# Kernel optimization log

Measured on AMD Instinct MI355X. Metric: run time of the kernel, lower is better.

The kernel has to match this reference:

```python
import jax, jax.numpy as jnp
import numpy as np

DIM = 768
NUM_SS = 8
INNER = DIM // 4  # s_ratio = 4 -> 192


def setup_inputs() -> dict:
    key = jax.random.key(0)
    ks = jax.random.split(key, 9)
    s = 0.02
    return {
        "x": jax.random.normal(ks[0], (16, 4096, DIM), dtype=jnp.float32),
        "Wq": jax.random.normal(ks[1], (DIM, DIM), dtype=jnp.float32) * s,
        "bq": jax.random.normal(ks[2], (DIM,), dtype=jnp.float32) * s,
        "Wk": jax.random.normal(ks[3], (DIM, NUM_SS * INNER), dtype=jnp.float32) * s,
        "bk": jax.random.normal(ks[4], (NUM_SS * INNER,), dtype=jnp.float32) * s,
        "Wv": jax.random.normal(ks[5], (DIM, DIM), dtype=jnp.float32) * s,
        "bv": jax.random.normal(ks[6], (DIM,), dtype=jnp.float32) * s,
        "Wss_out": jax.random.normal(ks[7], (INNER, DIM), dtype=jnp.float32) * s,
        "bss_out": jax.random.normal(ks[8], (DIM,), dtype=jnp.float32) * s,
    }


def reference(x, Wq, bq, Wk, bk, Wv, bv, Wss_out, bss_out):
    b = x.shape[0]
    ss_tokens = x[:, -NUM_SS:, :]          # [b, S, D]
    reg = x[:, :-NUM_SS, :]                # [b, T, D]
    x_v = reg @ Wv + bv                    # [b, T, D]
    x_q = reg @ Wq + bq                    # [b, T, D]
    x_k = reg @ Wk + bk                    # [b, T, S*I]
    # mean over regular tokens, reshape to one inner vector per ss token
    ss_update_ = jnp.mean(x_k, axis=1).reshape(b, NUM_SS, INNER)
    new_ss = ss_tokens + (ss_update_ @ Wss_out + bss_out)     # [b, S, D]
    scale = jnp.asarray(1.0 / np.sqrt(DIM), x.dtype)
    sim = jnp.einsum('btd,bsd->bts', x_q, new_ss) * scale     # [b, T, S]
    attn = jax.nn.softmax(sim, axis=-1)
    upd = jnp.einsum('bts,bsd->btd', attn, new_ss)            # [b, T, D]
    new_reg = jax.nn.relu(x_v + upd)
    return jnp.concatenate([new_reg, new_ss], axis=1)
```

## Files before the change

### kernel.cpp

```cpp
#include <hip/hip_runtime.h>
#include <hip/hip_bf16.h>

#define B_ 16
#define T_ 4096
#define TREG 4088
#define D_ 768
#define NSS 8
#define INNER_ 192
#define NK 1536
#define NCHUNK 128

typedef unsigned int u32;
typedef unsigned short u16;
typedef __attribute__((ext_vector_type(8))) short bf16x8;
typedef __attribute__((ext_vector_type(4))) float f32x4;

__device__ __forceinline__ u16 f2bf(float f) {
  union { __hip_bfloat16 h; u16 u; } cv;
  cv.h = __float2bfloat16(f);
  return cv.u;
}

__device__ __forceinline__ void load16_lds(const void* g, void* l) {
  __builtin_amdgcn_global_load_lds(
      (const __attribute__((address_space(1))) u32*)(unsigned long long)g,
      (__attribute__((address_space(3))) u32*)(u32)(unsigned long long)l,
      16, 0, 0);
}

__global__ __launch_bounds__(256) void k_wvt(const float* __restrict__ Wv,
                                             u16* __restrict__ wvT) {
  __shared__ float tile[16][17];
  int tx = threadIdx.x & 15, ty = threadIdx.x >> 4;
  int nb = blockIdx.x * 16, kb = blockIdx.y * 16;
  tile[ty][tx] = Wv[(size_t)(kb + ty) * D_ + nb + tx];
  __syncthreads();
  wvT[(size_t)(nb + ty) * D_ + kb + tx] = f2bf(tile[tx][ty]);
}

template <bool CONV>
__global__ __launch_bounds__(192) void k_conv_mean(const float* __restrict__ x,
                                                   u16* __restrict__ xb,
                                                   float* __restrict__ partials) {
  int b = blockIdx.y, tc = blockIdx.x, tid = threadIdx.x;
  const float4* xp = (const float4*)(x + (size_t)(b * T_ + tc * 32) * D_) + tid;
  ushort4* op = nullptr;
  if (CONV) op = ((ushort4*)(xb + (size_t)(b * T_ + tc * 32) * D_)) + tid;
  float s0 = 0, s1 = 0, s2 = 0, s3 = 0;
  int tbase = tc * 32;
#pragma unroll 4
  for (int tt = 0; tt < 32; ++tt) {
    float4 v = xp[(size_t)tt * 192];
    if (CONV) {
      ushort4 o;
      o.x = f2bf(v.x); o.y = f2bf(v.y); o.z = f2bf(v.z); o.w = f2bf(v.w);
      op[(size_t)tt * 192] = o;
    }
    if (tbase + tt < TREG) { s0 += v.x; s1 += v.y; s2 += v.z; s3 += v.w; }
  }
  float4 st; st.x = s0; st.y = s1; st.z = s2; st.w = s3;
  ((float4*)(partials + ((size_t)b * NCHUNK + tc) * D_))[tid] = st;
}

__global__ __launch_bounds__(256) void k_ssu(const float* __restrict__ partials,
                                             const float* __restrict__ Wk,
                                             const float* __restrict__ bk,
                                             float* __restrict__ ssu) {
  int b = blockIdx.y, tid = threadIdx.x;
  int n = blockIdx.x * 256 + tid;
  __shared__ float mv[D_];
  for (int d = tid; d < D_; d += 256) {
    const float* p = partials + (size_t)b * NCHUNK * D_ + d;
    float s = 0;
#pragma unroll 8
    for (int c = 0; c < NCHUNK; ++c) s += p[(size_t)c * D_];
    mv[d] = s * (1.0f / TREG);
  }
  __syncthreads();
  float a = bk[n];
#pragma unroll 8
  for (int d = 0; d < D_; ++d) a += mv[d] * Wk[(size_t)d * NK + n];
  ssu[(size_t)b * NK + n] = a;
}

__global__ __launch_bounds__(256) void k_nss(
    const float* __restrict__ x, const float* __restrict__ ssu,
    const float* __restrict__ Wss, const float* __restrict__ bss,
    const float* __restrict__ bq, float* __restrict__ out,
    float* __restrict__ nssf, u16* __restrict__ nssT, float* __restrict__ qb) {
  int s = blockIdx.x, b = blockIdx.y, tid = threadIdx.x;
  __shared__ float su[INNER_];
  __shared__ float qred[4];
  if (tid < INNER_) su[tid] = ssu[(size_t)b * NK + s * INNER_ + tid];
  __syncthreads();
  size_t xr = (size_t)(b * T_ + TREG + s) * D_;
  float a0 = x[xr + tid]       + bss[tid];
  float a1 = x[xr + tid + 256] + bss[tid + 256];
  float a2 = x[xr + tid + 512] + bss[tid + 512];
#pragma unroll 4
  for (int i = 0; i < INNER_; ++i) {
    float sv = su[i];
    const float* wr = Wss + (size_t)i * D_ + tid;
    a0 += sv * wr[0]; a1 += sv * wr[256]; a2 += sv * wr[512];
  }
  out[xr + tid] = a0; out[xr + tid + 256] = a1; out[xr + tid + 512] = a2;
  size_t nb = (size_t)(b * NSS + s) * D_;
  nssf[nb + tid] = a0; nssf[nb + tid + 256] = a1; nssf[nb + tid + 512] = a2;
  size_t tb = (size_t)b * D_;
  nssT[(tb + tid) * NSS + s] = f2bf(a0);
  nssT[(tb + tid + 256) * NSS + s] = f2bf(a1);
  nssT[(tb + tid + 512) * NSS + s] = f2bf(a2);
  float q = bq[tid] * a0 + bq[tid + 256] * a1 + bq[tid + 512] * a2;
#pragma unroll
  for (int o = 1; o < 64; o <<= 1) q += __shfl_xor(q, o, 64);
  if ((tid & 63) == 0) qred[tid >> 6] = q;
  __syncthreads();
  if (tid == 0) qb[b * NSS + s] = qred[0] + qred[1] + qred[2] + qred[3];
}

__global__ __launch_bounds__(256) void k_wqs(const float* __restrict__ Wq,
                                             const float* __restrict__ nssf,
                                             u16* __restrict__ wqsT) {
  __shared__ float nss[NSS * (D_ + 4)];
  int b = blockIdx.y, tid = threadIdx.x;
  int o = blockIdx.x * 256 + tid;
  int j = o >> 3, s = o & 7;
  for (int i = tid; i < NSS * D_; i += 256) {
    int s2 = i / D_, d2 = i - s2 * D_;
    nss[s2 * (D_ + 4) + d2] = nssf[(size_t)b * NSS * D_ + i];
  }
  __syncthreads();
  const float* wr = Wq + (size_t)j * D_;
  const float* nr = nss + s * (D_ + 4);
  float a = 0;
#pragma unroll 8
  for (int d = 0; d < D_; ++d) a += wr[d] * nr[d];
  wqsT[((size_t)b * NSS + s) * D_ + j] = f2bf(a);
}

template <bool ABF16>
__global__ __launch_bounds__(256, 3) void k_main(
    const u16* __restrict__ xb, const float* __restrict__ xf,
    const u16* __restrict__ wvT, const u16* __restrict__ wqsT,
    const u16* __restrict__ nssTg, const float* __restrict__ qb,
    const float* __restrict__ bv, float* __restrict__ out) {
  __shared__ uint4 ldsv[1800];
  u16* lds = (u16*)ldsv;
  u16* As = lds;
  u16* Bs = lds + 4096;
  u16* Ws = lds + 8192;

  const int tid = threadIdx.x;
  const int g = blockIdx.x;
  const int xcd = g & 7;
  const int li = g >> 3;
  const int nblk = li % 6;
  const int pair = li / 6;
  const int pid = pair * 8 + xcd;
  const int t0 = (pid & 31) * 128;
  const int b = pid >> 5;
  const int n0 = nblk * 128;

  const int wave = tid >> 6, lane = tid & 63;
  const int wy = wave >> 1, wx = wave & 1;
  const int lr = lane & 15, lq = lane >> 4;

  if (tid < 96) {
    for (int s = 0; s < 8; ++s)
      ((uint4*)(Ws + s * 776))[tid] =
          ((const uint4*)(wqsT + ((size_t)b * NSS + s) * D_))[tid];
  }

  f32x4 acc[4][4];
  f32x4 sacc[4];
#pragma unroll
  for (int i = 0; i < 4; ++i) {
    sacc[i] = f32x4{0.f, 0.f, 0.f, 0.f};
#pragma unroll
    for (int j = 0; j < 4; ++j) acc[i][j] = f32x4{0.f, 0.f, 0.f, 0.f};
  }

  const u16* Bg = wvT + (size_t)n0 * D_;
  const int c1 = tid + 256;
  const int ar0 = tid >> 2, ak0 = (tid & 3) * 8;
  const int ar1 = c1 >> 2, ak1 = (c1 & 3) * 8;

  for (int k0 = 0; k0 < D_; k0 += 32) {
    if constexpr (ABF16) {
      const u16* Ag = xb + (size_t)(b * T_ + t0) * D_;
      load16_lds(Ag + (size_t)ar0 * D_ + k0 + ak0, As + tid * 8);
      load16_lds(Ag + (size_t)ar1 * D_ + k0 + ak1, As + c1 * 8);
    } else {
      const float* Af = xf + (size_t)(b * T_ + t0) * D_;
      const float* p0 = Af + (size_t)ar0 * D_ + k0 + ak0;
      const float* p1 = Af + (size_t)ar1 * D_ + k0 + ak1;
      float4 a0 = *(const float4*)p0, a1 = *(const float4*)(p0 + 4);
      float4 a2 = *(const float4*)p1, a3 = *(const float4*)(p1 + 4);
      ushort4 w0, w1, w2, w3;
      w0.x = f2bf(a0.x); w0.y = f2bf(a0.y); w0.z = f2bf(a0.z); w0.w = f2bf(a0.w);
      w1.x = f2bf(a1.x); w1.y = f2bf(a1.y); w1.z = f2bf(a1.z); w1.w = f2bf(a1.w);
      w2.x = f2bf(a2.x); w2.y = f2bf(a2.y); w2.z = f2bf(a2.z); w2.w = f2bf(a2.w);
      w3.x = f2bf(a3.x); w3.y = f2bf(a3.y); w3.z = f2bf(a3.z); w3.w = f2bf(a3.w);
      *(ushort4*)(As + tid * 8) = w0; *(ushort4*)(As + tid * 8 + 4) = w1;
      *(ushort4*)(As + c1 * 8) = w2; *(ushort4*)(As + c1 * 8 + 4) = w3;
    }
    load16_lds(Bg + (size_t)ar0 * D_ + k0 + ak0, Bs + tid * 8);
    load16_lds(Bg + (size_t)ar1 * D_ + k0 + ak1, Bs + c1 * 8);
    __syncthreads();

    bf16x8 af[4], bfr[4], qf;
#pragma unroll
    for (int mt = 0; mt < 4; ++mt)
      af[mt] = *(const bf16x8*)(As + (wy * 64 + mt * 16 + lr) * 32 + lq * 8);
#pragma unroll
    for (int nt = 0; nt < 4; ++nt)
      bfr[nt] = *(const bf16x8*)(Bs + (wx * 64 + nt * 16 + lr) * 32 + lq * 8);
    qf = *(const bf16x8*)(Ws + (lr & 7) * 776 + k0 + lq * 8);
#pragma unroll
    for (int mt = 0; mt < 4; ++mt) {
#pragma unroll
      for (int nt = 0; nt < 4; ++nt)
        acc[mt][nt] = __builtin_amdgcn_mfma_f32_16x16x32_bf16(
            af[mt], bfr[nt], acc[mt][nt], 0, 0, 0);
      sacc[mt] = __builtin_amdgcn_mfma_f32_16x16x32_bf16(
          af[mt], qf, sacc[mt], 0, 0, 0);
    }
    __syncthreads();
  }

  u16* anb = lds;
  u16* nsl = lds + 4096;
  {
    uint4 z; z.x = z.y = z.z = z.w = 0;
    if (tid < 128) {
      uint4 v = *(const uint4*)(nssTg + ((size_t)b * D_ + n0 + tid) * NSS);
      *(uint4*)(nsl + tid * 32) = v;
      *(uint4*)(nsl + tid * 32 + 8) = z;
      *(uint4*)(nsl + tid * 32 + 16) = z;
      *(uint4*)(nsl + tid * 32 + 24) = z;
    } else {
      int r = tid - 128;
      *(uint4*)(anb + r * 32 + 8) = z;
      *(uint4*)(anb + r * 32 + 16) = z;
      *(uint4*)(anb + r * 32 + 24) = z;
    }
  }
  __syncthreads();

  const float scale = 0.03608439182435161f;
  const float qbias = (lr < 8) ? qb[b * NSS + lr] : 0.f;
#pragma unroll
  for (int mt = 0; mt < 4; ++mt) {
    f32x4 s4 = sacc[mt];
#pragma unroll
    for (int r = 0; r < 4; ++r) {
      float v = (lr < 8) ? (s4[r] + qbias) * scale : -1.0e30f;
      float mx = v;
      mx = fmaxf(mx, __shfl_xor(mx, 1, 16));
      mx = fmaxf(mx, __shfl_xor(mx, 2, 16));
      mx = fmaxf(mx, __shfl_xor(mx, 4, 16));
      float e = (lr < 8) ? __expf(v - mx) : 0.f;
      float sm = e;
      sm += __shfl_xor(sm, 1, 16);
      sm += __shfl_xor(sm, 2, 16);
      sm += __shfl_xor(sm, 4, 16);
      if (lr < 8) {
        float a = e / sm;
        anb[(wy * 64 + mt * 16 + lq * 4 + r) * 32 + lr] = f2bf(a);
      }
    }
  }
  __syncthreads();

  bf16x8 nf[4];
#pragma unroll
  for (int nt = 0; nt < 4; ++nt)
    nf[nt] = *(const bf16x8*)(nsl + (wx * 64 + nt * 16 + lr) * 32 + lq * 8);
#pragma unroll
  for (int mt = 0; mt < 4; ++mt) {
    bf16x8 afr = *(const bf16x8*)(anb + (wy * 64 + mt * 16 + lr) * 32 + lq * 8);
#pragma unroll
    for (int nt = 0; nt < 4; ++nt)
      acc[mt][nt] = __builtin_amdgcn_mfma_f32_16x16x32_bf16(
          afr, nf[nt], acc[mt][nt], 0, 0, 0);
  }

  float bvv[4];
#pragma unroll
  for (int nt = 0; nt < 4; ++nt) bvv[nt] = bv[n0 + wx * 64 + nt * 16 + lr];
#pragma unroll
  for (int mt = 0; mt < 4; ++mt) {
    int trow = wy * 64 + mt * 16 + lq * 4;
#pragma unroll
    for (int r = 0; r < 4; ++r) {
      int token = t0 + trow + r;
      if (token < TREG) {
        float* op = out + ((size_t)b * T_ + token) * D_ + n0 + wx * 64;
#pragma unroll
        for (int nt = 0; nt < 4; ++nt)
          op[nt * 16 + lr] = fmaxf(acc[mt][nt][r] + bvv[nt], 0.f);
      }
    }
  }
}

extern "C" void kernel_launch(void* const* d_in, const int* in_sizes, int n_in,
                              void* d_out, int out_size, void* d_ws, size_t ws_size,
                              hipStream_t stream) {
  (void)in_sizes; (void)n_in; (void)out_size;
  const float* x   = (const float*)d_in[0];
  const float* Wq  = (const float*)d_in[1];
  const float* bq  = (const float*)d_in[2];
  const float* Wk  = (const float*)d_in[3];
  const float* bk  = (const float*)d_in[4];
  const float* Wv  = (const float*)d_in[5];
  const float* bv  = (const float*)d_in[6];
  const float* Wss = (const float*)d_in[7];
  const float* bss = (const float*)d_in[8];
  float* out = (float*)d_out;

  const size_t SZ_XB   = (size_t)B_ * T_ * D_ * 2;
  const size_t SZ_WVT  = (size_t)D_ * D_ * 2;
  const size_t SZ_PART = (size_t)B_ * NCHUNK * D_ * 4;
  const size_t SZ_SSU  = (size_t)B_ * NK * 4;
  const size_t SZ_NSSF = (size_t)B_ * NSS * D_ * 4;
  const size_t SZ_NSST = (size_t)B_ * D_ * NSS * 2;
  const size_t SZ_QB   = (size_t)B_ * NSS * 4;
  const size_t SZ_WQS  = (size_t)B_ * NSS * D_ * 2;
  const size_t SMALL = SZ_WVT + SZ_PART + SZ_SSU + SZ_NSSF + SZ_NSST + SZ_QB + SZ_WQS;
  const size_t FULL = SZ_XB + SMALL;
  const bool big = ws_size >= FULL;

  char* ws = (char*)d_ws;
  size_t off = big ? SZ_XB : 0;
  u16*   xb    = (u16*)ws;
  u16*   wvT   = (u16*)(ws + off);   off += SZ_WVT;
  float* parts = (float*)(ws + off); off += SZ_PART;
  float* ssu   = (float*)(ws + off); off += SZ_SSU;
  float* nssf  = (float*)(ws + off); off += SZ_NSSF;
  u16*   nssT  = (u16*)(ws + off);   off += SZ_NSST;
  float* qbb   = (float*)(ws + off); off += SZ_QB;
  u16*   wqsT  = (u16*)(ws + off);   off += SZ_WQS;

  k_wvt<<<dim3(48, 48), 256, 0, stream>>>(Wv, wvT);
  if (big)
    k_conv_mean<true><<<dim3(NCHUNK, 16), 192, 0, stream>>>(x, xb, parts);
  else
    k_conv_mean<false><<<dim3(NCHUNK, 16), 192, 0, stream>>>(x, nullptr, parts);
  k_ssu<<<dim3(6, 16), 256, 0, stream>>>(parts, Wk, bk, ssu);
  k_nss<<<dim3(NSS, 16), 256, 0, stream>>>(x, ssu, Wss, bss, bq, out, nssf, nssT, qbb);
  k_wqs<<<dim3(24, 16), 256, 0, stream>>>(Wq, nssf, wqsT);
  if (big)
    k_main<true><<<3072, 256, 0, stream>>>(xb, x, wvT, wqsT, nssT, qbb, bv, out);
  else
    k_main<false><<<3072, 256, 0, stream>>>(nullptr, x, wvT, wqsT, nssT, qbb, bv, out);
}
```

Measured before the change: 607.2 us.

## Double-buffer main GEMM LDS tiles with XOR swizzle and streamed Wq·ss tiles

```diff
diff --git a/kernel.cpp b/kernel.cpp
--- a/kernel.cpp
+++ b/kernel.cpp
@@ -139,16 +139,17 @@
 }
 
 template <bool ABF16>
-__global__ __launch_bounds__(256, 3) void k_main(
+__global__ __launch_bounds__(256, 4) void k_main(
     const u16* __restrict__ xb, const float* __restrict__ xf,
     const u16* __restrict__ wvT, const u16* __restrict__ wqsT,
     const u16* __restrict__ nssTg, const float* __restrict__ qb,
     const float* __restrict__ bv, float* __restrict__ out) {
-  __shared__ uint4 ldsv[1800];
+  __shared__ uint4 ldsv[2112];
   u16* lds = (u16*)ldsv;
-  u16* As = lds;
-  u16* Bs = lds + 4096;
-  u16* Ws = lds + 8192;
+  u16* As0 = lds;
+  u16* Bs0 = lds + 4096;
+  u16* As1 = lds + 8448;
+  u16* Bs1 = lds + 12544;
 
   const int tid = threadIdx.x;
   const int g = blockIdx.x;
@@ -165,11 +166,17 @@
   const int wy = wave >> 1, wx = wave & 1;
   const int lr = lane & 15, lq = lane >> 4;
 
-  if (tid < 96) {
-    for (int s = 0; s < 8; ++s)
-      ((uint4*)(Ws + s * 776))[tid] =
-          ((const uint4*)(wqsT + ((size_t)b * NSS + s) * D_))[tid];
-  }
+  const int ar = tid >> 2;
+  const int agc = (tid & 3) ^ ((ar >> 1) & 3);
+  const int fch = (lq ^ ((lr >> 1) & 3)) * 8;
+
+  const u16* Bg = wvT + (size_t)n0 * D_;
+  const u16* Qg = wqsT + (size_t)b * NSS * D_;
+  const int qs = tid >> 2;
+  const int qgc = (tid & 3) ^ ((qs >> 1) & 3);
+
+  const u16* Ag16 = ABF16 ? (xb + (size_t)(b * T_ + t0) * D_) : nullptr;
+  const float* Agf = ABF16 ? nullptr : (xf + (size_t)(b * T_ + t0) * D_);
 
   f32x4 acc[4][4];
   f32x4 sacc[4];
@@ -180,20 +187,14 @@
     for (int j = 0; j < 4; ++j) acc[i][j] = f32x4{0.f, 0.f, 0.f, 0.f};
   }
 
-  const u16* Bg = wvT + (size_t)n0 * D_;
-  const int c1 = tid + 256;
-  const int ar0 = tid >> 2, ak0 = (tid & 3) * 8;
-  const int ar1 = c1 >> 2, ak1 = (c1 & 3) * 8;
-
-  for (int k0 = 0; k0 < D_; k0 += 32) {
+  auto STAGE = [&](u16* As, u16* Bs, int k0) {
     if constexpr (ABF16) {
-      const u16* Ag = xb + (size_t)(b * T_ + t0) * D_;
-      load16_lds(Ag + (size_t)ar0 * D_ + k0 + ak0, As + tid * 8);
-      load16_lds(Ag + (size_t)ar1 * D_ + k0 + ak1, As + c1 * 8);
+      load16_lds(Ag16 + (size_t)ar * D_ + k0 + agc * 8, As + tid * 8);
+      load16_lds(Ag16 + (size_t)(ar + 64) * D_ + k0 + agc * 8,
+                 As + (tid + 256) * 8);
     } else {
-      const float* Af = xf + (size_t)(b * T_ + t0) * D_;
-      const float* p0 = Af + (size_t)ar0 * D_ + k0 + ak0;
-      const float* p1 = Af + (size_t)ar1 * D_ + k0 + ak1;
+      const float* p0 = Agf + (size_t)ar * D_ + k0 + agc * 8;
+      const float* p1 = Agf + (size_t)(ar + 64) * D_ + k0 + agc * 8;
       float4 a0 = *(const float4*)p0, a1 = *(const float4*)(p0 + 4);
       float4 a2 = *(const float4*)p1, a3 = *(const float4*)(p1 + 4);
       ushort4 w0, w1, w2, w3;
@@ -202,20 +203,24 @@
       w2.x = f2bf(a2.x); w2.y = f2bf(a2.y); w2.z = f2bf(a2.z); w2.w = f2bf(a2.w);
       w3.x = f2bf(a3.x); w3.y = f2bf(a3.y); w3.z = f2bf(a3.z); w3.w = f2bf(a3.w);
       *(ushort4*)(As + tid * 8) = w0; *(ushort4*)(As + tid * 8 + 4) = w1;
-      *(ushort4*)(As + c1 * 8) = w2; *(ushort4*)(As + c1 * 8 + 4) = w3;
-    }
-    load16_lds(Bg + (size_t)ar0 * D_ + k0 + ak0, Bs + tid * 8);
-    load16_lds(Bg + (size_t)ar1 * D_ + k0 + ak1, Bs + c1 * 8);
-    __syncthreads();
-
+      *(ushort4*)(As + (tid + 256) * 8) = w2;
+      *(ushort4*)(As + (tid + 256) * 8 + 4) = w3;
+    }
+    load16_lds(Bg + (size_t)ar * D_ + k0 + agc * 8, Bs + tid * 8);
+    load16_lds(Bg + (size_t)(ar + 64) * D_ + k0 + agc * 8, Bs + (tid + 256) * 8);
+    if (tid < 32)
+      load16_lds(Qg + (size_t)qs * D_ + k0 + qgc * 8, Bs + 4096 + tid * 8);
+  };
+
+  auto COMPUTE = [&](const u16* As, const u16* Bs) {
     bf16x8 af[4], bfr[4], qf;
 #pragma unroll
     for (int mt = 0; mt < 4; ++mt)
-      af[mt] = *(const bf16x8*)(As + (wy * 64 + mt * 16 + lr) * 32 + lq * 8);
+      af[mt] = *(const bf16x8*)(As + (wy * 64 + mt * 16 + lr) * 32 + fch);
 #pragma unroll
     for (int nt = 0; nt < 4; ++nt)
-      bfr[nt] = *(const bf16x8*)(Bs + (wx * 64 + nt * 16 + lr) * 32 + lq * 8);
-    qf = *(const bf16x8*)(Ws + (lr & 7) * 776 + k0 + lq * 8);
+      bfr[nt] = *(const bf16x8*)(Bs + (wx * 64 + nt * 16 + lr) * 32 + fch);
+    qf = *(const bf16x8*)(Bs + (128 + (lr & 7)) * 32 + fch);
 #pragma unroll
     for (int mt = 0; mt < 4; ++mt) {
 #pragma unroll
@@ -225,6 +230,17 @@
       sacc[mt] = __builtin_amdgcn_mfma_f32_16x16x32_bf16(
           af[mt], qf, sacc[mt], 0, 0, 0);
     }
+  };
+
+  STAGE(As0, Bs0, 0);
+  __syncthreads();
+#pragma unroll 1
+  for (int k0 = 0; k0 < D_; k0 += 64) {
+    STAGE(As1, Bs1, k0 + 32);
+    COMPUTE(As0, Bs0);
+    __syncthreads();
+    if (k0 + 64 < D_) STAGE(As0, Bs0, k0 + 64);
+    COMPUTE(As1, Bs1);
     __syncthreads();
   }
 
@@ -234,12 +250,14 @@
     uint4 z; z.x = z.y = z.z = z.w = 0;
     if (tid < 128) {
       uint4 v = *(const uint4*)(nssTg + ((size_t)b * D_ + n0 + tid) * NSS);
-      *(uint4*)(nsl + tid * 32) = v;
-      *(uint4*)(nsl + tid * 32 + 8) = z;
-      *(uint4*)(nsl + tid * 32 + 16) = z;
-      *(uint4*)(nsl + tid * 32 + 24) = z;
+      int sw = ((tid >> 1) & 3) * 8;
+      *(uint4*)(nsl + tid * 32 + sw) = v;
+      *(uint4*)(nsl + tid * 32 + (sw ^ 8)) = z;
+      *(uint4*)(nsl + tid * 32 + (sw ^ 16)) = z;
+      *(uint4*)(nsl + tid * 32 + (sw ^ 24)) = z;
     } else {
       int r = tid - 128;
+      *(uint4*)(anb + r * 32) = z;
       *(uint4*)(anb + r * 32 + 8) = z;
       *(uint4*)(anb + r * 32 + 16) = z;
       *(uint4*)(anb + r * 32 + 24) = z;
@@ -266,7 +284,8 @@
       sm += __shfl_xor(sm, 4, 16);
       if (lr < 8) {
         float a = e / sm;
-        anb[(wy * 64 + mt * 16 + lq * 4 + r) * 32 + lr] = f2bf(a);
+        int row = wy * 64 + mt * 16 + lq * 4 + r;
+        anb[row * 32 + ((row >> 1) & 3) * 8 + lr] = f2bf(a);
       }
     }
   }
@@ -275,10 +294,11 @@
   bf16x8 nf[4];
 #pragma unroll
   for (int nt = 0; nt < 4; ++nt)
-    nf[nt] = *(const bf16x8*)(nsl + (wx * 64 + nt * 16 + lr) * 32 + lq * 8);
+    nf[nt] = *(const bf16x8*)(nsl + (wx * 64 + nt * 16 + lr) * 32 + fch);
 #pragma unroll
   for (int mt = 0; mt < 4; ++mt) {
-    bf16x8 afr = *(const bf16x8*)(anb + (wy * 64 + mt * 16 + lr) * 32 + lq * 8);
+    bf16x8 afr =
+        *(const bf16x8*)(anb + (wy * 64 + mt * 16 + lr) * 32 + fch);
 #pragma unroll
     for (int nt = 0; nt < 4; ++nt)
       acc[mt][nt] = __builtin_amdgcn_mfma_f32_16x16x32_bf16(
```

New measurement: 629.0 us. +3.6%, slower.
